# Kernel tuning notes

Measured on AMD Instinct MI355X. Metric: run time of the kernel, lower is better.

Reference implementation:

```python
import jax, jax.numpy as jnp
import numpy as np

EPS = 1e-6
NEG_SLOPE = 0.2


def _basis(J):
    # J: [B,N,E,3] -> R: [B,N,E,3(k: U,V,J rows),3(xyz comp)]
    nJ = J / (jnp.linalg.norm(J, axis=-1, keepdims=True) + EPS)
    sub = nJ[..., :2]
    u_z = -(sub[..., 0] ** 2 + sub[..., 1] ** 2) / (nJ[..., 2] + EPS)
    U = jnp.concatenate([sub, u_z[..., None]], axis=-1)
    U = U / (jnp.linalg.norm(U, axis=-1, keepdims=True) + EPS)
    V = jnp.cross(U, nJ)
    return jnp.stack([U, V, nJ], axis=-2)


def _complex_linear(X, J, A, Bw, Cw):
    R = _basis(J)                                   # [B,N,E,3,3], R[...,k,i]
    RtX = jnp.einsum('bneki,bnek->bnei', R, X)      # (R^T X)_i = sum_k R[k,i] X_k
    # rrtx(i, s) has component k equal to R[...,k,i] * s
    a_term = R[..., 0] * RtX[..., 0:1] + R[..., 1] * RtX[..., 1:2]
    b_term = R[..., 1] * RtX[..., 0:1] - R[..., 0] * RtX[..., 1:2]
    c_term = R[..., 2] * RtX[..., 2:3]
    Y = (jnp.einsum('fe,bnei->bnfi', A, a_term)
         + jnp.einsum('fe,bnei->bnfi', Bw, b_term)
         + jnp.einsum('fe,bnei->bnfi', Cw, c_term))
    return Y                                        # [B,N,F,3]


def _vn_leaky_relu(x, W, negative_slope):
    # x: [B,F,3,N]; W: [F,F] torch Linear weight (out,in)
    d = jnp.einsum('gf,bfin->bgin', W, x)
    dot = jnp.sum(x * d, axis=2, keepdims=True)
    d_norm_sq = jnp.sum(d * d, axis=2, keepdims=True)
    neg_branch = x - (dot / (d_norm_sq + EPS)) * d
    lin = jnp.where(dot >= 0, x, neg_branch)
    return negative_slope * x + (1.0 - negative_slope) * lin


def setup_inputs() -> dict:
    key = jax.random.key(0)
    kX, kJ, kA, kB, kC, kW = jax.random.split(key, 6)
    B, N, E, F = 16, 1024, 256, 256
    X = jax.random.normal(kX, (B, N, E, 3), dtype=jnp.float32)
    J = jax.random.normal(kJ, (B, N, E, 3), dtype=jnp.float32)
    A = jax.random.normal(kA, (F, E), dtype=jnp.float32)
    Bw = jax.random.normal(kB, (F, E), dtype=jnp.float32)
    Cw = jax.random.normal(kC, (F, E), dtype=jnp.float32)
    W = jax.random.normal(kW, (F, F), dtype=jnp.float32) * (1.0 / np.sqrt(F))
    return {"X": X, "J": J, "A": A, "Bw": Bw, "Cw": Cw, "W": W, "device": 0}


def reference(X, J, A, Bw, Cw, W, device):
    Y = _complex_linear(X, J, A, Bw, Cw)            # [B,N,F,3]
    x = jnp.transpose(Y, (0, 2, 3, 1))              # [B,F,3,N]
    return _vn_leaky_relu(x, W, NEG_SLOPE)
```

## Files before the change

### kernel.cpp

```cpp
#include <hip/hip_runtime.h>

typedef __attribute__((ext_vector_type(8))) _Float16 half8;
typedef __attribute__((ext_vector_type(4))) _Float16 half4v;
typedef __attribute__((ext_vector_type(4))) float f32x4;
typedef float f32x4u __attribute__((ext_vector_type(4), aligned(4)));
typedef float f32x2u __attribute__((ext_vector_type(2), aligned(4)));

#define EPSF 1e-6f

__device__ __forceinline__ void glds16(const void* g, void* l) {
    __builtin_amdgcn_global_load_lds(
        (const __attribute__((address_space(1))) unsigned*)g,
        (__attribute__((address_space(3))) unsigned*)l, 16, 0, 0);
}
__device__ __forceinline__ unsigned short h2u(_Float16 h) {
    union { _Float16 h; unsigned short u; } c; c.h = h; return c.u;
}

__global__ __launch_bounds__(256) void prep_kernel(
    const float* __restrict__ A, const float* __restrict__ Bw,
    const float* __restrict__ Cw, const float* __restrict__ W,
    _Float16* __restrict__ Mh, _Float16* __restrict__ Wh)
{
    int f = blockIdx.x, e = threadIdx.x;
    Mh[f * 768 + e]       = (_Float16)A[f * 256 + e];
    Mh[f * 768 + 256 + e] = (_Float16)Bw[f * 256 + e];
    Mh[f * 768 + 512 + e] = (_Float16)Cw[f * 256 + e];
    Wh[f * 256 + e]       = (_Float16)W[f * 256 + e];
}

__global__ __launch_bounds__(512, 4) void fused_kernel(
    const float* __restrict__ X, const float* __restrict__ Jp,
    const _Float16* __restrict__ Mh, const _Float16* __restrict__ Wh,
    float* __restrict__ out)
{
    extern __shared__ char lds[];
    const int T_OFF = 49152;
    int tid = threadIdx.x;
    int b  = blockIdx.x >> 5;
    int n0 = (blockIdx.x & 31) * 32;

    int l = tid & 63, lr = l & 15, lq = l >> 4;
    int w = tid >> 6, wc = w & 1, wf = w >> 1;
    int nl = tid >> 4, ep = tid & 15;

    size_t pb0 = ((size_t)((b * 1024 + n0 + nl) * 256) + 2 * ep) * 3;

    auto loadXJ = [&](int eb, float* xs, float* js) {
        size_t pb = pb0 + (size_t)eb * 96;
        f32x4u xa = *(const f32x4u*)(X + pb);
        f32x2u xb = *(const f32x2u*)(X + pb + 4);
        f32x4u ja = *(const f32x4u*)(Jp + pb);
        f32x2u jb = *(const f32x2u*)(Jp + pb + 4);
        xs[0]=xa[0]; xs[1]=xa[1]; xs[2]=xa[2]; xs[3]=xa[3]; xs[4]=xb[0]; xs[5]=xb[1];
        js[0]=ja[0]; js[1]=ja[1]; js[2]=ja[2]; js[3]=ja[3]; js[4]=jb[0]; js[5]=jb[1];
    };

    auto stageA = [&](int eb) {
        #pragma unroll
        for (int h = 0; h < 6; ++h) {
            int m = h * 512 + tid;
            int t = m >> 10, fr = (m >> 2) & 255, slot = m & 3;
            size_t go = ((size_t)fr * 768 + t * 256 + eb * 32
                         + ((slot ^ ((fr >> 1) & 3)) * 8)) * 2;
            glds16((const char*)Mh + go, lds + m * 16);
        }
    };

    auto computeT = [&](const float* xs, const float* js) {
        unsigned short hv[2][9];
        #pragma unroll
        for (int p = 0; p < 2; ++p) {
            float x0 = xs[3*p], x1 = xs[3*p+1], x2 = xs[3*p+2];
            float j0 = js[3*p], j1 = js[3*p+1], j2 = js[3*p+2];
            float jj  = j0*j0 + j1*j1 + j2*j2;
            float rn  = __builtin_amdgcn_rcpf(__builtin_amdgcn_sqrtf(jj) + EPSF);
            float nj0 = j0*rn, nj1 = j1*rn, nj2 = j2*rn;
            float s2  = nj0*nj0 + nj1*nj1;
            float uz  = -s2 * __builtin_amdgcn_rcpf(nj2 + EPSF);
            float ru  = __builtin_amdgcn_rcpf(__builtin_amdgcn_sqrtf(s2 + uz*uz) + EPSF);
            float u0 = nj0*ru, u1 = nj1*ru, u2 = uz*ru;
            float v0 = u1*nj2 - u2*nj1;
            float v1 = u2*nj0 - u0*nj2;
            float v2 = u0*nj1 - u1*nj0;
            float r0 = u0*x0 + v0*x1 + nj0*x2;
            float r1 = u1*x0 + v1*x1 + nj1*x2;
            float r2 = u2*x0 + v2*x1 + nj2*x2;
            hv[p][0] = h2u((_Float16)(u0*r0 + u1*r1));
            hv[p][1] = h2u((_Float16)(v0*r0 + v1*r1));
            hv[p][2] = h2u((_Float16)(nj0*r0 + nj1*r1));
            hv[p][3] = h2u((_Float16)(u1*r0 - u0*r1));
            hv[p][4] = h2u((_Float16)(v1*r0 - v0*r1));
            hv[p][5] = h2u((_Float16)(nj1*r0 - nj0*r1));
            hv[p][6] = h2u((_Float16)(u2*r2));
            hv[p][7] = h2u((_Float16)(v2*r2));
            hv[p][8] = h2u((_Float16)(nj2*r2));
        }
        #pragma unroll
        for (int s = 0; s < 9; ++s) {
            int t = s / 3, i = s % 3;
            unsigned pk = (unsigned)hv[0][s] | ((unsigned)hv[1][s] << 16);
            *(unsigned*)(lds + T_OFF + (t * 96 + i * 32 + nl) * 80 + ep * 4) = pk;
        }
    };

    f32x4 acc[3][4] = {};
    float xs[6], js[6];
    loadXJ(0, xs, js);

    for (int eb = 0; eb < 8; ++eb) {
        __syncthreads();
        stageA(eb);
        computeT(xs, js);
        __syncthreads();
        if (eb < 7) loadXJ(eb + 1, xs, js);

        #pragma unroll
        for (int t = 0; t < 3; ++t) {
            half8 af[4], bf[3];
            #pragma unroll
            for (int mi = 0; mi < 4; ++mi) {
                int f = wf * 64 + mi * 16 + lr;
                af[mi] = *(const half8*)(lds + t * 16384 + f * 64
                                         + ((lq ^ ((f >> 1) & 3)) * 16));
            }
            #pragma unroll
            for (int bi = 0; bi < 3; ++bi) {
                int cr = wc * 48 + bi * 16 + lr;
                bf[bi] = *(const half8*)(lds + T_OFF + (t * 96 + cr) * 80 + lq * 16);
            }
            #pragma unroll
            for (int bi = 0; bi < 3; ++bi)
                #pragma unroll
                for (int mi = 0; mi < 4; ++mi)
                    acc[bi][mi] = __builtin_amdgcn_mfma_f32_16x16x32_f16(af[mi], bf[bi], acc[bi][mi], 0, 0, 0);
        }
    }

    __syncthreads();
    #pragma unroll
    for (int bi = 0; bi < 3; ++bi) {
        int c = wc * 48 + bi * 16 + lr;
        #pragma unroll
        for (int mi = 0; mi < 4; ++mi) {
            int fb2 = (wf * 64 + mi * 16 + lq * 4) * 2;
            f32x4 v = acc[bi][mi];
            half4v p;
            p.x = (_Float16)v[0]; p.y = (_Float16)v[1];
            p.z = (_Float16)v[2]; p.w = (_Float16)v[3];
            *(half4v*)(lds + c * 512 + (fb2 ^ ((c & 7) << 4))) = p;
        }
    }

    int nh = w & 1, gw = w >> 1;
    half8 wreg[2][4];
    #pragma unroll
    for (int gf = 0; gf < 4; ++gf) {
        int g = gw * 64 + gf * 16 + lr;
        wreg[0][gf] = *(const half8*)(Wh + (size_t)g * 256 + lq * 8);
    }
    __syncthreads();

    f32x4 acc2[3][4] = {};
    #pragma unroll
    for (int kt = 0; kt < 8; ++kt) {
        if (kt < 7) {
            #pragma unroll
            for (int gf = 0; gf < 4; ++gf) {
                int g = gw * 64 + gf * 16 + lr;
                wreg[(kt + 1) & 1][gf] =
                    *(const half8*)(Wh + (size_t)g * 256 + (kt + 1) * 32 + lq * 8);
            }
        }
        half8 yf[3];
        #pragma unroll
        for (int ci = 0; ci < 3; ++ci) {
            int c = ci * 32 + nh * 16 + lr;
            yf[ci] = *(const half8*)(lds + c * 512
                                     + ((kt * 64 + lq * 16) ^ ((c & 7) << 4)));
        }
        #pragma unroll
        for (int ci = 0; ci < 3; ++ci)
            #pragma unroll
            for (int gf = 0; gf < 4; ++gf)
                acc2[ci][gf] = __builtin_amdgcn_mfma_f32_16x16x32_f16(
                    yf[ci], wreg[kt & 1][gf], acc2[ci][gf], 0, 0, 0);
    }

    #pragma unroll
    for (int gf = 0; gf < 4; ++gf) {
        int g = gw * 64 + gf * 16 + lr;
        f32x4 o[3];
        #pragma unroll
        for (int r = 0; r < 4; ++r) {
            float xv[3];
            #pragma unroll
            for (int ci = 0; ci < 3; ++ci) {
                int c = ci * 32 + nh * 16 + lq * 4 + r;
                xv[ci] = (float)*(const _Float16*)(lds + c * 512
                                 + ((g * 2) ^ ((c & 7) << 4)));
            }
            float d0 = acc2[0][gf][r], d1 = acc2[1][gf][r], d2 = acc2[2][gf][r];
            float dot = xv[0] * d0 + xv[1] * d1 + xv[2] * d2;
            float dn  = d0 * d0 + d1 * d1 + d2 * d2;
            float sc  = dot / (dn + EPSF);
            bool pos  = dot >= 0.0f;
            float l0 = pos ? xv[0] : fmaf(-sc, d0, xv[0]);
            float l1 = pos ? xv[1] : fmaf(-sc, d1, xv[1]);
            float l2 = pos ? xv[2] : fmaf(-sc, d2, xv[2]);
            o[0][r] = fmaf(0.8f, l0, 0.2f * xv[0]);
            o[1][r] = fmaf(0.8f, l1, 0.2f * xv[1]);
            o[2][r] = fmaf(0.8f, l2, 0.2f * xv[2]);
        }
        int nb = n0 + nh * 16 + lq * 4;
        #pragma unroll
        for (int i = 0; i < 3; ++i)
            *(f32x4*)(out + ((size_t)(b * 256 + g) * 3 + i) * 1024 + nb) = o[i];
    }
}

extern "C" void kernel_launch(void* const* d_in, const int* in_sizes, int n_in,
                              void* d_out, int out_size, void* d_ws, size_t ws_size,
                              hipStream_t stream)
{
    const float* X  = (const float*)d_in[0];
    const float* J  = (const float*)d_in[1];
    const float* A  = (const float*)d_in[2];
    const float* Bw = (const float*)d_in[3];
    const float* Cw = (const float*)d_in[4];
    const float* W  = (const float*)d_in[5];
    float* out = (float*)d_out;

    char* ws = (char*)d_ws;
    _Float16* Mh = (_Float16*)ws;
    _Float16* Wh = (_Float16*)(ws + 393216);

    (void)hipFuncSetAttribute((const void*)fused_kernel,
                              hipFuncAttributeMaxDynamicSharedMemorySize, 72192);

    hipLaunchKernelGGL(prep_kernel,  dim3(256), dim3(256), 0, stream,
                       A, Bw, Cw, W, Mh, Wh);
    hipLaunchKernelGGL(fused_kernel, dim3(512), dim3(512), 72192, stream,
                       X, J, Mh, Wh, out);
}
```

Measured before the change: 58.56 us.

## Load weight MFMA fragments directly from global into registers with prefetch

Drops LDS staging of the fp16 weight matrix through global_load_lds. Each wave now reads its A-operand fragments straight from global memory (held in L2) into registers. The load for the next t-step is issued before the current MFMAs, using a ping-pong pair of register buffers. This is meant to remove LDS write/read traffic and some synchronisation work, and it shrinks dynamic LDS to 48KB. In exchange, fragments are loaded redundantly across waves and the kernel becomes exposed to global-load latency and higher register pressure.

```diff
diff --git a/kernel.cpp b/kernel.cpp
--- a/kernel.cpp
+++ b/kernel.cpp
@@ -8,11 +8,6 @@
 
 #define EPSF 1e-6f
 
-__device__ __forceinline__ void glds16(const void* g, void* l) {
-    __builtin_amdgcn_global_load_lds(
-        (const __attribute__((address_space(1))) unsigned*)g,
-        (__attribute__((address_space(3))) unsigned*)l, 16, 0, 0);
-}
 __device__ __forceinline__ unsigned short h2u(_Float16 h) {
     union { _Float16 h; unsigned short u; } c; c.h = h; return c.u;
 }
@@ -35,7 +30,6 @@
     float* __restrict__ out)
 {
     extern __shared__ char lds[];
-    const int T_OFF = 49152;
     int tid = threadIdx.x;
     int b  = blockIdx.x >> 5;
     int n0 = (blockIdx.x & 31) * 32;
@@ -54,17 +48,6 @@
         f32x2u jb = *(const f32x2u*)(Jp + pb + 4);
         xs[0]=xa[0]; xs[1]=xa[1]; xs[2]=xa[2]; xs[3]=xa[3]; xs[4]=xb[0]; xs[5]=xb[1];
         js[0]=ja[0]; js[1]=ja[1]; js[2]=ja[2]; js[3]=ja[3]; js[4]=jb[0]; js[5]=jb[1];
-    };
-
-    auto stageA = [&](int eb) {
-        #pragma unroll
-        for (int h = 0; h < 6; ++h) {
-            int m = h * 512 + tid;
-            int t = m >> 10, fr = (m >> 2) & 255, slot = m & 3;
-            size_t go = ((size_t)fr * 768 + t * 256 + eb * 32
-                         + ((slot ^ ((fr >> 1) & 3)) * 8)) * 2;
-            glds16((const char*)Mh + go, lds + m * 16);
-        }
     };
 
     auto computeT = [&](const float* xs, const float* js) {
@@ -100,41 +83,51 @@
         for (int s = 0; s < 9; ++s) {
             int t = s / 3, i = s % 3;
             unsigned pk = (unsigned)hv[0][s] | ((unsigned)hv[1][s] << 16);
-            *(unsigned*)(lds + T_OFF + (t * 96 + i * 32 + nl) * 80 + ep * 4) = pk;
+            *(unsigned*)(lds + (t * 96 + i * 32 + nl) * 80 + ep * 4) = pk;
         }
     };
 
     f32x4 acc[3][4] = {};
+    half8 afA[4], afB[4];
     float xs[6], js[6];
-    loadXJ(0, xs, js);
-
-    for (int eb = 0; eb < 8; ++eb) {
+
+    auto loadAf = [&](half8* dst, int neb, int nt) {
+        #pragma unroll
+        for (int mi = 0; mi < 4; ++mi) {
+            int f = wf * 64 + mi * 16 + lr;
+            dst[mi] = *(const half8*)(Mh + (size_t)f * 768 + nt * 256 + neb * 32 + lq * 8);
+        }
+    };
+    auto tstep = [&](const half8* use, half8* nxt, int t, int neb, int nt, bool doload) {
+        if (doload) loadAf(nxt, neb, nt);
+        half8 bf[3];
+        #pragma unroll
+        for (int bi = 0; bi < 3; ++bi) {
+            int cr = wc * 48 + bi * 16 + lr;
+            bf[bi] = *(const half8*)(lds + (t * 96 + cr) * 80 + lq * 16);
+        }
+        #pragma unroll
+        for (int bi = 0; bi < 3; ++bi)
+            #pragma unroll
+            for (int mi = 0; mi < 4; ++mi)
+                acc[bi][mi] = __builtin_amdgcn_mfma_f32_16x16x32_f16(use[mi], bf[bi], acc[bi][mi], 0, 0, 0);
+    };
+    auto ebbody = [&](int eb, half8* P, half8* Q, bool last) {
         __syncthreads();
-        stageA(eb);
         computeT(xs, js);
         __syncthreads();
-        if (eb < 7) loadXJ(eb + 1, xs, js);
-
-        #pragma unroll
-        for (int t = 0; t < 3; ++t) {
-            half8 af[4], bf[3];
-            #pragma unroll
-            for (int mi = 0; mi < 4; ++mi) {
-                int f = wf * 64 + mi * 16 + lr;
-                af[mi] = *(const half8*)(lds + t * 16384 + f * 64
-                                         + ((lq ^ ((f >> 1) & 3)) * 16));
-            }
-            #pragma unroll
-            for (int bi = 0; bi < 3; ++bi) {
-                int cr = wc * 48 + bi * 16 + lr;
-                bf[bi] = *(const half8*)(lds + T_OFF + (t * 96 + cr) * 80 + lq * 16);
-            }
-            #pragma unroll
-            for (int bi = 0; bi < 3; ++bi)
-                #pragma unroll
-                for (int mi = 0; mi < 4; ++mi)
-                    acc[bi][mi] = __builtin_amdgcn_mfma_f32_16x16x32_f16(af[mi], bf[bi], acc[bi][mi], 0, 0, 0);
-        }
+        if (!last) loadXJ(eb + 1, xs, js);
+        tstep(P, Q, 0, eb, 1, true);
+        tstep(Q, P, 1, eb, 2, true);
+        tstep(P, Q, 2, eb + 1, 0, !last);
+    };
+
+    loadXJ(0, xs, js);
+    loadAf(afA, 0, 0);
+    for (int ep2 = 0; ep2 < 4; ++ep2) {
+        int e0 = ep2 * 2;
+        ebbody(e0,     afA, afB, false);
+        ebbody(e0 + 1, afB, afA, e0 + 1 == 7);
     }
 
     __syncthreads();
@@ -236,10 +229,10 @@
     _Float16* Wh = (_Float16*)(ws + 393216);
 
     (void)hipFuncSetAttribute((const void*)fused_kernel,
-                              hipFuncAttributeMaxDynamicSharedMemorySize, 72192);
+                              hipFuncAttributeMaxDynamicSharedMemorySize, 49152);
 
     hipLaunchKernelGGL(prep_kernel,  dim3(256), dim3(256), 0, stream,
                        A, Bw, Cw, W, Mh, Wh);
-    hipLaunchKernelGGL(fused_kernel, dim3(512), dim3(512), 72192, stream,
+    hipLaunchKernelGGL(fused_kernel, dim3(512), dim3(512), 49152, stream,
                        X, J, Mh, Wh, out);
 }
```

After: 86.40 us. +47.5%, slower.

## Software-pipeline GEMM with double-buffered A slices and T tiles

Applied to the files above, without the earlier changes.

Splits the per-eb staging of the three weight slices into per-t async global-to-LDS loads into two ping-pong 16KB buffers, and double-buffers the T tile so the next block's T compute overlaps current MFMA work. Each stage's load is issued before the MFMA on the previous buffer, so load latency is meant to hide behind matrix work rather than stall at a barrier. It adds more barriers per iteration (three instead of two) and raises LDS to about 77KB, which may limit the occupancy requested by the launch bounds.

```diff
diff --git a/kernel.cpp b/kernel.cpp
--- a/kernel.cpp
+++ b/kernel.cpp
@@ -35,7 +35,7 @@
     float* __restrict__ out)
 {
     extern __shared__ char lds[];
-    const int T_OFF = 49152;
+    const int T_OFF = 32768;
     int tid = threadIdx.x;
     int b  = blockIdx.x >> 5;
     int n0 = (blockIdx.x & 31) * 32;
@@ -56,18 +56,18 @@
         js[0]=ja[0]; js[1]=ja[1]; js[2]=ja[2]; js[3]=ja[3]; js[4]=jb[0]; js[5]=jb[1];
     };
 
-    auto stageA = [&](int eb) {
-        #pragma unroll
-        for (int h = 0; h < 6; ++h) {
+    auto stageT = [&](int p, int eb, int t) {
+        #pragma unroll
+        for (int h = 0; h < 2; ++h) {
             int m = h * 512 + tid;
-            int t = m >> 10, fr = (m >> 2) & 255, slot = m & 3;
+            int fr = m >> 2, slot = m & 3;
             size_t go = ((size_t)fr * 768 + t * 256 + eb * 32
                          + ((slot ^ ((fr >> 1) & 3)) * 8)) * 2;
-            glds16((const char*)Mh + go, lds + m * 16);
-        }
-    };
-
-    auto computeT = [&](const float* xs, const float* js) {
+            glds16((const char*)Mh + go, lds + p * 16384 + m * 16);
+        }
+    };
+
+    auto computeT = [&](const float* xs, const float* js, int tbase) {
         unsigned short hv[2][9];
         #pragma unroll
         for (int p = 0; p < 2; ++p) {
@@ -100,44 +100,55 @@
         for (int s = 0; s < 9; ++s) {
             int t = s / 3, i = s % 3;
             unsigned pk = (unsigned)hv[0][s] | ((unsigned)hv[1][s] << 16);
-            *(unsigned*)(lds + T_OFF + (t * 96 + i * 32 + nl) * 80 + ep * 4) = pk;
+            *(unsigned*)(lds + tbase + (t * 96 + i * 32 + nl) * 80 + ep * 4) = pk;
         }
     };
 
     f32x4 acc[3][4] = {};
+
+    auto mstep = [&](int ap, int eb, int t) {
+        half8 af[4], bf[3];
+        const char* Ab = lds + ap * 16384;
+        const char* Tb = lds + T_OFF + (eb & 1) * 23040;
+        #pragma unroll
+        for (int mi = 0; mi < 4; ++mi) {
+            int f = wf * 64 + mi * 16 + lr;
+            af[mi] = *(const half8*)(Ab + f * 64 + ((lq ^ ((f >> 1) & 3)) * 16));
+        }
+        #pragma unroll
+        for (int bi = 0; bi < 3; ++bi) {
+            int cr = wc * 48 + bi * 16 + lr;
+            bf[bi] = *(const half8*)(Tb + (t * 96 + cr) * 80 + lq * 16);
+        }
+        #pragma unroll
+        for (int bi = 0; bi < 3; ++bi)
+            #pragma unroll
+            for (int mi = 0; mi < 4; ++mi)
+                acc[bi][mi] = __builtin_amdgcn_mfma_f32_16x16x32_f16(af[mi], bf[bi], acc[bi][mi], 0, 0, 0);
+    };
+
     float xs[6], js[6];
     loadXJ(0, xs, js);
+    computeT(xs, js, T_OFF);
+    stageT(0, 0, 0);
+    loadXJ(1, xs, js);
+    __syncthreads();
 
     for (int eb = 0; eb < 8; ++eb) {
+        int s0 = 3 * eb;
+        stageT((s0 + 1) & 1, eb, 1);
+        if (eb < 7) computeT(xs, js, T_OFF + ((eb + 1) & 1) * 23040);
+        mstep(s0 & 1, eb, 0);
         __syncthreads();
-        stageA(eb);
-        computeT(xs, js);
+        stageT((s0 + 2) & 1, eb, 2);
+        mstep((s0 + 1) & 1, eb, 1);
         __syncthreads();
-        if (eb < 7) loadXJ(eb + 1, xs, js);
-
-        #pragma unroll
-        for (int t = 0; t < 3; ++t) {
-            half8 af[4], bf[3];
-            #pragma unroll
-            for (int mi = 0; mi < 4; ++mi) {
-                int f = wf * 64 + mi * 16 + lr;
-                af[mi] = *(const half8*)(lds + t * 16384 + f * 64
-                                         + ((lq ^ ((f >> 1) & 3)) * 16));
-            }
-            #pragma unroll
-            for (int bi = 0; bi < 3; ++bi) {
-                int cr = wc * 48 + bi * 16 + lr;
-                bf[bi] = *(const half8*)(lds + T_OFF + (t * 96 + cr) * 80 + lq * 16);
-            }
-            #pragma unroll
-            for (int bi = 0; bi < 3; ++bi)
-                #pragma unroll
-                for (int mi = 0; mi < 4; ++mi)
-                    acc[bi][mi] = __builtin_amdgcn_mfma_f32_16x16x32_f16(af[mi], bf[bi], acc[bi][mi], 0, 0, 0);
-        }
-    }
-
-    __syncthreads();
+        if (eb < 7) stageT((s0 + 3) & 1, eb + 1, 0);
+        if (eb < 6) loadXJ(eb + 2, xs, js);
+        mstep((s0 + 2) & 1, eb, 2);
+        __syncthreads();
+    }
+
     #pragma unroll
     for (int bi = 0; bi < 3; ++bi) {
         int c = wc * 48 + bi * 16 + lr;
@@ -236,10 +247,10 @@
     _Float16* Wh = (_Float16*)(ws + 393216);
 
     (void)hipFuncSetAttribute((const void*)fused_kernel,
-                              hipFuncAttributeMaxDynamicSharedMemorySize, 72192);
+                              hipFuncAttributeMaxDynamicSharedMemorySize, 78848);
 
     hipLaunchKernelGGL(prep_kernel,  dim3(256), dim3(256), 0, stream,
                        A, Bw, Cw, W, Mh, Wh);
-    hipLaunchKernelGGL(fused_kernel, dim3(512), dim3(512), 72192, stream,
+    hipLaunchKernelGGL(fused_kernel, dim3(512), dim3(512), 78848, stream,
                        X, J, Mh, Wh, out);
 }
```

After: 58.25 us. No clear change (-0.5%).

## Double the N tile, double-buffer weight staging, compute T directly in registers

Applied to the files above, without the earlier changes.

Each block now covers 64 points instead of 32, which halves the grid and doubles reuse of the fp16 weight tiles staged per block. The weight slice for the next E-block is prefetched into a second LDS buffer while the current one is consumed, leaving one barrier per iteration. Each lane computes its rotated-basis terms straight into MFMA B-fragment registers, removing the LDS T staging area. In exchange the block uses more registers and LDS (occupancy bound lowered to 2) and the grid has only 256 blocks, which may underfill the GPU.

```diff
diff --git a/kernel.cpp b/kernel.cpp
--- a/kernel.cpp
+++ b/kernel.cpp
@@ -4,7 +4,6 @@
 typedef __attribute__((ext_vector_type(4))) _Float16 half4v;
 typedef __attribute__((ext_vector_type(4))) float f32x4;
 typedef float f32x4u __attribute__((ext_vector_type(4), aligned(4)));
-typedef float f32x2u __attribute__((ext_vector_type(2), aligned(4)));
 
 #define EPSF 1e-6f
 
@@ -12,9 +11,6 @@
     __builtin_amdgcn_global_load_lds(
         (const __attribute__((address_space(1))) unsigned*)g,
         (__attribute__((address_space(3))) unsigned*)l, 16, 0, 0);
-}
-__device__ __forceinline__ unsigned short h2u(_Float16 h) {
-    union { _Float16 h; unsigned short u; } c; c.h = h; return c.u;
 }
 
 __global__ __launch_bounds__(256) void prep_kernel(
@@ -29,50 +25,56 @@
     Wh[f * 256 + e]       = (_Float16)W[f * 256 + e];
 }
 
-__global__ __launch_bounds__(512, 4) void fused_kernel(
+__global__ __launch_bounds__(512, 2) void fused_kernel(
     const float* __restrict__ X, const float* __restrict__ Jp,
     const _Float16* __restrict__ Mh, const _Float16* __restrict__ Wh,
     float* __restrict__ out)
 {
     extern __shared__ char lds[];
-    const int T_OFF = 49152;
     int tid = threadIdx.x;
-    int b  = blockIdx.x >> 5;
-    int n0 = (blockIdx.x & 31) * 32;
+    int b  = blockIdx.x >> 4;
+    int n0 = (blockIdx.x & 15) * 64;
 
     int l = tid & 63, lr = l & 15, lq = l >> 4;
-    int w = tid >> 6, wc = w & 1, wf = w >> 1;
-    int nl = tid >> 4, ep = tid & 15;
-
-    size_t pb0 = ((size_t)((b * 1024 + n0 + nl) * 256) + 2 * ep) * 3;
-
-    auto loadXJ = [&](int eb, float* xs, float* js) {
-        size_t pb = pb0 + (size_t)eb * 96;
-        f32x4u xa = *(const f32x4u*)(X + pb);
-        f32x2u xb = *(const f32x2u*)(X + pb + 4);
-        f32x4u ja = *(const f32x4u*)(Jp + pb);
-        f32x2u jb = *(const f32x2u*)(Jp + pb + 4);
-        xs[0]=xa[0]; xs[1]=xa[1]; xs[2]=xa[2]; xs[3]=xa[3]; xs[4]=xb[0]; xs[5]=xb[1];
-        js[0]=ja[0]; js[1]=ja[1]; js[2]=ja[2]; js[3]=ja[3]; js[4]=jb[0]; js[5]=jb[1];
-    };
-
-    auto stageA = [&](int eb) {
+    int w = tid >> 6, wf = w & 1, wc = w >> 1;
+
+    auto stageEB = [&](int p, int eb) {
         #pragma unroll
         for (int h = 0; h < 6; ++h) {
             int m = h * 512 + tid;
             int t = m >> 10, fr = (m >> 2) & 255, slot = m & 3;
             size_t go = ((size_t)fr * 768 + t * 256 + eb * 32
                          + ((slot ^ ((fr >> 1) & 3)) * 8)) * 2;
-            glds16((const char*)Mh + go, lds + m * 16);
+            glds16((const char*)Mh + go, lds + p * 49152 + m * 16);
         }
     };
 
-    auto computeT = [&](const float* xs, const float* js) {
-        unsigned short hv[2][9];
-        #pragma unroll
-        for (int p = 0; p < 2; ++p) {
-            float x0 = xs[3*p], x1 = xs[3*p+1], x2 = xs[3*p+2];
-            float j0 = js[3*p], j1 = js[3*p+1], j2 = js[3*p+2];
+    f32x4 acc[3][8] = {};
+
+    size_t pb0 = ((size_t)((b * 1024 + n0 + wc * 16 + lr) * 256) + lq * 8) * 3;
+
+    stageEB(0, 0);
+    __syncthreads();
+
+    for (int eb = 0; eb < 8; ++eb) {
+        int cur = eb & 1;
+        if (eb < 7) stageEB(cur ^ 1, eb + 1);
+
+        size_t pb = pb0 + (size_t)eb * 96;
+        float xa[24], ja[24];
+        #pragma unroll
+        for (int h = 0; h < 6; ++h) {
+            f32x4u xv = *(const f32x4u*)(X + pb + h * 4);
+            f32x4u jv = *(const f32x4u*)(Jp + pb + h * 4);
+            xa[h*4+0] = xv[0]; xa[h*4+1] = xv[1]; xa[h*4+2] = xv[2]; xa[h*4+3] = xv[3];
+            ja[h*4+0] = jv[0]; ja[h*4+1] = jv[1]; ja[h*4+2] = jv[2]; ja[h*4+3] = jv[3];
+        }
+
+        half8 bf[3][3];
+        #pragma unroll
+        for (int j = 0; j < 8; ++j) {
+            float x0 = xa[3*j], x1 = xa[3*j+1], x2 = xa[3*j+2];
+            float j0 = ja[3*j], j1 = ja[3*j+1], j2 = ja[3*j+2];
             float jj  = j0*j0 + j1*j1 + j2*j2;
             float rn  = __builtin_amdgcn_rcpf(__builtin_amdgcn_sqrtf(jj) + EPSF);
             float nj0 = j0*rn, nj1 = j1*rn, nj2 = j2*rn;
@@ -86,65 +88,43 @@
             float r0 = u0*x0 + v0*x1 + nj0*x2;
             float r1 = u1*x0 + v1*x1 + nj1*x2;
             float r2 = u2*x0 + v2*x1 + nj2*x2;
-            hv[p][0] = h2u((_Float16)(u0*r0 + u1*r1));
-            hv[p][1] = h2u((_Float16)(v0*r0 + v1*r1));
-            hv[p][2] = h2u((_Float16)(nj0*r0 + nj1*r1));
-            hv[p][3] = h2u((_Float16)(u1*r0 - u0*r1));
-            hv[p][4] = h2u((_Float16)(v1*r0 - v0*r1));
-            hv[p][5] = h2u((_Float16)(nj1*r0 - nj0*r1));
-            hv[p][6] = h2u((_Float16)(u2*r2));
-            hv[p][7] = h2u((_Float16)(v2*r2));
-            hv[p][8] = h2u((_Float16)(nj2*r2));
-        }
-        #pragma unroll
-        for (int s = 0; s < 9; ++s) {
-            int t = s / 3, i = s % 3;
-            unsigned pk = (unsigned)hv[0][s] | ((unsigned)hv[1][s] << 16);
-            *(unsigned*)(lds + T_OFF + (t * 96 + i * 32 + nl) * 80 + ep * 4) = pk;
-        }
-    };
-
-    f32x4 acc[3][4] = {};
-    float xs[6], js[6];
-    loadXJ(0, xs, js);
-
-    for (int eb = 0; eb < 8; ++eb) {
+            bf[0][0][j] = (_Float16)(u0*r0 + u1*r1);
+            bf[0][1][j] = (_Float16)(v0*r0 + v1*r1);
+            bf[0][2][j] = (_Float16)(nj0*r0 + nj1*r1);
+            bf[1][0][j] = (_Float16)(u1*r0 - u0*r1);
+            bf[1][1][j] = (_Float16)(v1*r0 - v0*r1);
+            bf[1][2][j] = (_Float16)(nj1*r0 - nj0*r1);
+            bf[2][0][j] = (_Float16)(u2*r2);
+            bf[2][1][j] = (_Float16)(v2*r2);
+            bf[2][2][j] = (_Float16)(nj2*r2);
+        }
+
+        #pragma unroll
+        for (int t = 0; t < 3; ++t) {
+            half8 af[8];
+            #pragma unroll
+            for (int mi = 0; mi < 8; ++mi) {
+                int f = wf * 128 + mi * 16 + lr;
+                af[mi] = *(const half8*)(lds + cur * 49152 + t * 16384 + f * 64
+                                         + ((lq ^ ((f >> 1) & 3)) * 16));
+            }
+            #pragma unroll
+            for (int i = 0; i < 3; ++i)
+                #pragma unroll
+                for (int mi = 0; mi < 8; ++mi)
+                    acc[i][mi] = __builtin_amdgcn_mfma_f32_16x16x32_f16(
+                        af[mi], bf[t][i], acc[i][mi], 0, 0, 0);
+        }
         __syncthreads();
-        stageA(eb);
-        computeT(xs, js);
-        __syncthreads();
-        if (eb < 7) loadXJ(eb + 1, xs, js);
-
-        #pragma unroll
-        for (int t = 0; t < 3; ++t) {
-            half8 af[4], bf[3];
-            #pragma unroll
-            for (int mi = 0; mi < 4; ++mi) {
-                int f = wf * 64 + mi * 16 + lr;
-                af[mi] = *(const half8*)(lds + t * 16384 + f * 64
-                                         + ((lq ^ ((f >> 1) & 3)) * 16));
-            }
-            #pragma unroll
-            for (int bi = 0; bi < 3; ++bi) {
-                int cr = wc * 48 + bi * 16 + lr;
-                bf[bi] = *(const half8*)(lds + T_OFF + (t * 96 + cr) * 80 + lq * 16);
-            }
-            #pragma unroll
-            for (int bi = 0; bi < 3; ++bi)
-                #pragma unroll
-                for (int mi = 0; mi < 4; ++mi)
-                    acc[bi][mi] = __builtin_amdgcn_mfma_f32_16x16x32_f16(af[mi], bf[bi], acc[bi][mi], 0, 0, 0);
-        }
-    }
-
-    __syncthreads();
-    #pragma unroll
-    for (int bi = 0; bi < 3; ++bi) {
-        int c = wc * 48 + bi * 16 + lr;
-        #pragma unroll
-        for (int mi = 0; mi < 4; ++mi) {
-            int fb2 = (wf * 64 + mi * 16 + lq * 4) * 2;
-            f32x4 v = acc[bi][mi];
+    }
+
+    #pragma unroll
+    for (int i = 0; i < 3; ++i) {
+        int c = i * 64 + wc * 16 + lr;
+        #pragma unroll
+        for (int mi = 0; mi < 8; ++mi) {
+            int fb2 = (wf * 128 + mi * 16 + lq * 4) * 2;
+            f32x4 v = acc[i][mi];
             half4v p;
             p.x = (_Float16)v[0]; p.y = (_Float16)v[1];
             p.z = (_Float16)v[2]; p.w = (_Float16)v[3];
@@ -161,7 +141,7 @@
     }
     __syncthreads();
 
-    f32x4 acc2[3][4] = {};
+    f32x4 acc2[3][2][4] = {};
     #pragma unroll
     for (int kt = 0; kt < 8; ++kt) {
         if (kt < 7) {
@@ -172,51 +152,52 @@
                     *(const half8*)(Wh + (size_t)g * 256 + (kt + 1) * 32 + lq * 8);
             }
         }
-        half8 yf[3];
-        #pragma unroll
-        for (int ci = 0; ci < 3; ++ci) {
-            int c = ci * 32 + nh * 16 + lr;
-            yf[ci] = *(const half8*)(lds + c * 512
-                                     + ((kt * 64 + lq * 16) ^ ((c & 7) << 4)));
-        }
         #pragma unroll
         for (int ci = 0; ci < 3; ++ci)
             #pragma unroll
-            for (int gf = 0; gf < 4; ++gf)
-                acc2[ci][gf] = __builtin_amdgcn_mfma_f32_16x16x32_f16(
-                    yf[ci], wreg[kt & 1][gf], acc2[ci][gf], 0, 0, 0);
-    }
-
-    #pragma unroll
-    for (int gf = 0; gf < 4; ++gf) {
-        int g = gw * 64 + gf * 16 + lr;
-        f32x4 o[3];
-        #pragma unroll
-        for (int r = 0; r < 4; ++r) {
-            float xv[3];
-            #pragma unroll
-            for (int ci = 0; ci < 3; ++ci) {
-                int c = ci * 32 + nh * 16 + lq * 4 + r;
-                xv[ci] = (float)*(const _Float16*)(lds + c * 512
-                                 + ((g * 2) ^ ((c & 7) << 4)));
-            }
-            float d0 = acc2[0][gf][r], d1 = acc2[1][gf][r], d2 = acc2[2][gf][r];
-            float dot = xv[0] * d0 + xv[1] * d1 + xv[2] * d2;
-            float dn  = d0 * d0 + d1 * d1 + d2 * d2;
-            float sc  = dot / (dn + EPSF);
-            bool pos  = dot >= 0.0f;
-            float l0 = pos ? xv[0] : fmaf(-sc, d0, xv[0]);
-            float l1 = pos ? xv[1] : fmaf(-sc, d1, xv[1]);
-            float l2 = pos ? xv[2] : fmaf(-sc, d2, xv[2]);
-            o[0][r] = fmaf(0.8f, l0, 0.2f * xv[0]);
-            o[1][r] = fmaf(0.8f, l1, 0.2f * xv[1]);
-            o[2][r] = fmaf(0.8f, l2, 0.2f * xv[2]);
-        }
-        int nb = n0 + nh * 16 + lq * 4;
-        #pragma unroll
-        for (int i = 0; i < 3; ++i)
-            *(f32x4*)(out + ((size_t)(b * 256 + g) * 3 + i) * 1024 + nb) = o[i];
-    }
+            for (int nc = 0; nc < 2; ++nc) {
+                int c = ci * 64 + nh * 32 + nc * 16 + lr;
+                half8 yf = *(const half8*)(lds + c * 512
+                             + ((kt * 64 + lq * 16) ^ ((c & 7) << 4)));
+                #pragma unroll
+                for (int gf = 0; gf < 4; ++gf)
+                    acc2[ci][nc][gf] = __builtin_amdgcn_mfma_f32_16x16x32_f16(
+                        yf, wreg[kt & 1][gf], acc2[ci][nc][gf], 0, 0, 0);
+            }
+    }
+
+    #pragma unroll
+    for (int nc = 0; nc < 2; ++nc)
+        #pragma unroll
+        for (int gf = 0; gf < 4; ++gf) {
+            int g = gw * 64 + gf * 16 + lr;
+            f32x4 o[3];
+            #pragma unroll
+            for (int r = 0; r < 4; ++r) {
+                float xv[3];
+                #pragma unroll
+                for (int ci = 0; ci < 3; ++ci) {
+                    int c = ci * 64 + nh * 32 + nc * 16 + lq * 4 + r;
+                    xv[ci] = (float)*(const _Float16*)(lds + c * 512
+                                     + ((g * 2) ^ ((c & 7) << 4)));
+                }
+                float d0 = acc2[0][nc][gf][r], d1 = acc2[1][nc][gf][r], d2 = acc2[2][nc][gf][r];
+                float dot = xv[0] * d0 + xv[1] * d1 + xv[2] * d2;
+                float dn  = d0 * d0 + d1 * d1 + d2 * d2;
+                float sc  = dot / (dn + EPSF);
+                bool pos  = dot >= 0.0f;
+                float l0 = pos ? xv[0] : fmaf(-sc, d0, xv[0]);
+                float l1 = pos ? xv[1] : fmaf(-sc, d1, xv[1]);
+                float l2 = pos ? xv[2] : fmaf(-sc, d2, xv[2]);
+                o[0][r] = fmaf(0.8f, l0, 0.2f * xv[0]);
+                o[1][r] = fmaf(0.8f, l1, 0.2f * xv[1]);
+                o[2][r] = fmaf(0.8f, l2, 0.2f * xv[2]);
+            }
+            int nb = n0 + nh * 32 + nc * 16 + lq * 4;
+            #pragma unroll
+            for (int i = 0; i < 3; ++i)
+                *(f32x4*)(out + ((size_t)(b * 256 + g) * 3 + i) * 1024 + nb) = o[i];
+        }
 }
 
 extern "C" void kernel_launch(void* const* d_in, const int* in_sizes, int n_in,
@@ -236,10 +217,10 @@
     _Float16* Wh = (_Float16*)(ws + 393216);
 
     (void)hipFuncSetAttribute((const void*)fused_kernel,
-                              hipFuncAttributeMaxDynamicSharedMemorySize, 72192);
+                              hipFuncAttributeMaxDynamicSharedMemorySize, 98304);
 
     hipLaunchKernelGGL(prep_kernel,  dim3(256), dim3(256), 0, stream,
                        A, Bw, Cw, W, Mh, Wh);
-    hipLaunchKernelGGL(fused_kernel, dim3(512), dim3(512), 72192, stream,
+    hipLaunchKernelGGL(fused_kernel, dim3(256), dim3(512), 98304, stream,
                        X, J, Mh, Wh, out);
 }
```

Result: slower. 71.45 us (+22.0%).
